# Kernel tuning notes

Hardware: AMD Instinct MI355X
Metric: run time of the kernel (lower is better)

The kernel has to match this reference:

```python
import jax, jax.numpy as jnp
import numpy as np
from jax import lax

NL = 4        # n_layers
V = 32000     # vocab_size
D = 768       # embedding_dim (d_model)
L = 2048      # seq_len
B = 1         # batch
E = 1536      # d_inner = expand * d_model
N = 8         # d_state
R = 48        # dt_rank = ceil(768/16)
K = 3         # d_conv


def rmsnorm(x, w, eps=1e-6):
    return x * w * lax.rsqrt(jnp.mean(x * x, axis=-1, keepdims=True) + eps)


def causal_dwconv(x, w, b):
    # depthwise causal conv1d; x: (B,L,E), w: (K,E), b: (E,)
    xp = jnp.pad(x, ((0, 0), (K - 1, 0), (0, 0)))
    y = sum(xp[:, k:k + x.shape[1], :] * w[k] for k in range(K))
    return y + b


def selective_scan(dt, A, Bm, C, u):
    # dt,u: (B,L,E); A: (E,N); Bm,C: (B,L,N)
    dA = jnp.exp(dt[..., None] * A)                      # (B,L,E,N)
    dBu = dt[..., None] * Bm[:, :, None, :] * u[..., None]  # (B,L,E,N)

    def step(h, xs):
        a, bu, c = xs
        h = a * h + bu                                   # (B,E,N)
        return h, jnp.einsum('ben,bn->be', h, c)

    h0 = jnp.zeros((u.shape[0], E, N), u.dtype)
    _, ys = lax.scan(step, h0, (dA.swapaxes(0, 1), dBu.swapaxes(0, 1), C.swapaxes(0, 1)))
    return ys.swapaxes(0, 1)                             # (B,L,E)


def mamba_block(x, Wi, bi, cw, cb, Wx, Wdt, bdt, Alog, Dsk, Wo, bo):
    xz = x @ Wi + bi                                     # (B,L,2E)
    u, res = jnp.split(xz, 2, axis=-1)
    u = jax.nn.silu(causal_dwconv(u, cw, cb))
    dbl = u @ Wx                                         # (B,L,R+2N)
    dt, Bm, C = dbl[..., :R], dbl[..., R:R + N], dbl[..., R + N:]
    dt = jax.nn.softplus(dt @ Wdt + bdt)                 # (B,L,E)
    A = -jnp.exp(Alog)                                   # (E,N)
    y = selective_scan(dt, A, Bm, C, u) + u * Dsk
    y = y * jax.nn.silu(res)
    return y @ Wo + bo


def setup_inputs() -> dict:
    key = jax.random.key(0)
    ks = jax.random.split(key, 10)
    s = 0.02
    return {
        'inputs': jax.random.randint(ks[0], (B, L), 0, V),
        'emb': jax.random.normal(ks[1], (V, D), jnp.float32) * s,
        'W_in': jax.random.normal(ks[2], (NL, D, 2 * E), jnp.float32) * s,
        'b_in': jnp.zeros((NL, 2 * E), jnp.float32),
        'conv_w': jax.random.normal(ks[3], (NL, K, E), jnp.float32) * s,
        'conv_b': jnp.zeros((NL, E), jnp.float32),
        'W_x': jax.random.normal(ks[4], (NL, E, R + 2 * N), jnp.float32) * s,
        'W_dt': jax.random.normal(ks[5], (NL, R, E), jnp.float32) * s,
        'b_dt': jax.random.normal(ks[6], (NL, E), jnp.float32) * s,
        'A_log': jnp.tile(jnp.log(jnp.arange(1, N + 1, dtype=jnp.float32)), (NL, E, 1)),
        'D_skip': jnp.ones((NL, E), jnp.float32),
        'W_out': jax.random.normal(ks[7], (NL, E, D), jnp.float32) * s,
        'b_out': jnp.zeros((NL, D), jnp.float32),
        'norm_w': jnp.ones((NL, D), jnp.float32),
        'normf_w': jnp.ones((D,), jnp.float32),
        'W_lm': jax.random.normal(ks[8], (D, V), jnp.float32) * s,
    }


def reference(inputs, emb, W_in, b_in, conv_w, conv_b, W_x, W_dt, b_dt, A_log, D_skip, W_out, b_out, norm_w, normf_w, W_lm):
    x = emb[inputs]                                      # (B,L,D)
    for i in range(NL):
        x = x + mamba_block(rmsnorm(x, norm_w[i]), W_in[i], b_in[i], conv_w[i], conv_b[i],
                            W_x[i], W_dt[i], b_dt[i], A_log[i], D_skip[i], W_out[i], b_out[i])
    x = rmsnorm(x, normf_w)
    return x @ W_lm                                      # logits (B,L,V)
```

## Files before the change

### kernel.cpp

```cpp
#include <hip/hip_runtime.h>
#include <hip/hip_bf16.h>
#include <cstdint>
#include <cstddef>

#define L_SEQ 2048
#define DIM   768
#define EDIM  1536
#define NLAY  4
#define NST   8
#define RNK   48
#define VOC   32000
#define NCH   128
#define CHS   16
#define TT    8

typedef __bf16 bf16x8 __attribute__((ext_vector_type(8)));
typedef float  f32x4  __attribute__((ext_vector_type(4)));

typedef __attribute__((address_space(3))) void lds_void;
typedef const __attribute__((address_space(1))) void gbl_void;

__device__ __forceinline__ void gld_lds16(const void* g, void* l) {
    __builtin_amdgcn_global_load_lds((gbl_void*)g, (lds_void*)l, 16, 0, 0);
}

__device__ __forceinline__ float bf2f(__hip_bfloat16 v) { return __bfloat162float(v); }

__global__ __launch_bounds__(256)
void prep_k(const float* __restrict__ W_in, const float* __restrict__ W_out,
            const float* __restrict__ W_lm, const float* __restrict__ W_x,
            __hip_bfloat16* __restrict__ WiT, __hip_bfloat16* __restrict__ WoT,
            __hip_bfloat16* __restrict__ WlmT, __hip_bfloat16* __restrict__ WxT)
{
    __shared__ float tile[32][33];
    int bid = blockIdx.x;
    const float* src; __hip_bfloat16* dst;
    int R, C, c0, r0;
    if (bid < 9216) {
        const int lz = bid / 2304, rem = bid % 2304;
        R = 768; C = 3072; c0 = (rem % 96) * 32; r0 = (rem / 96) * 32;
        src = W_in + (size_t)lz * 768 * 3072; dst = WiT + (size_t)lz * 3072 * 768;
    } else if (bid < 9216 + 4608) {
        bid -= 9216;
        const int lz = bid / 1152, rem = bid % 1152;
        R = 1536; C = 768; c0 = (rem % 24) * 32; r0 = (rem / 24) * 32;
        src = W_out + (size_t)lz * 1536 * 768; dst = WoT + (size_t)lz * 768 * 1536;
    } else if (bid < 9216 + 4608 + 24000) {
        bid -= 9216 + 4608;
        R = 768; C = 32000; c0 = (bid % 1000) * 32; r0 = (bid / 1000) * 32;
        src = W_lm; dst = WlmT;
    } else {
        bid -= 9216 + 4608 + 24000;
        const int lz = bid / 96, rem = bid % 96;
        R = 1536; C = 64; c0 = (rem % 2) * 32; r0 = (rem / 2) * 32;
        src = W_x + (size_t)lz * 1536 * 64; dst = WxT + (size_t)lz * 64 * 1536;
    }
    const int tx = threadIdx.x & 31;
    const int ty = threadIdx.x >> 5;
#pragma unroll
    for (int j = 0; j < 32; j += 8)
        tile[ty + j][tx] = src[(size_t)(r0 + ty + j) * C + c0 + tx];
    __syncthreads();
#pragma unroll
    for (int j = 0; j < 32; j += 8)
        dst[(size_t)(c0 + ty + j) * R + r0 + tx] = __float2bfloat16(tile[tx][ty + j]);
}

template<bool EMB>
__global__ __launch_bounds__(256)
void rmsnorm4_k(const float* __restrict__ src, const float* __restrict__ w,
                __hip_bfloat16* __restrict__ out,
                const int* __restrict__ ids, const float* __restrict__ emb,
                float* __restrict__ xcopy)
{
    const int row  = blockIdx.x * 4 + (threadIdx.x >> 6);
    const int lane = threadIdx.x & 63;
    const float* xr;
    if constexpr (EMB) xr = emb + (size_t)ids[row] * DIM;
    else               xr = src + (size_t)row * DIM;
    float v[12];
    float s = 0.f;
#pragma unroll
    for (int j = 0; j < 12; ++j) { v[j] = xr[lane + j * 64]; s += v[j] * v[j]; }
#pragma unroll
    for (int m = 32; m >= 1; m >>= 1) s += __shfl_xor(s, m, 64);
    const float sc = rsqrtf(s * (1.0f / DIM) + 1e-6f);
    __hip_bfloat16* o = out + (size_t)row * DIM;
#pragma unroll
    for (int j = 0; j < 12; ++j)
        o[lane + j * 64] = __float2bfloat16(v[j] * w[lane + j * 64] * sc);
    if constexpr (EMB) {
        float* xc = xcopy + (size_t)row * DIM;
#pragma unroll
        for (int j = 0; j < 12; ++j) xc[lane + j * 64] = v[j];
    }
}

template<int EPI, int BM, int BN, int BK, typename OT>
__global__ __launch_bounds__(256)
void gemm_bf16(const __hip_bfloat16* __restrict__ A,
               const __hip_bfloat16* __restrict__ BT,
               const float* __restrict__ bias,
               OT* __restrict__ C,
               int M, int N, int K)
{
    constexpr int WM = BM / 2, WN = BN / 2;
    constexpr int MF = WM / 16, NF = WN / 16;
    constexpr int AOPS = BM * BK * 2 / 4096;
    constexpr int BOPS = BN * BK * 2 / 4096;
    constexpr int SOPS = AOPS + BOPS;
    static_assert(SOPS == 3 || SOPS == 4, "vmcnt literal");

    __shared__ __hip_bfloat16 As[2][BM * BK];
    __shared__ __hip_bfloat16 Bs[2][BN * BK];

    const int tid  = threadIdx.x;
    const int lane = tid & 63, wid = tid >> 6;
    const int wr = wid >> 1, wc = wid & 1;

    const int nwg = gridDim.x;
    int wg = blockIdx.x;
    if ((nwg & 7) == 0) wg = (wg & 7) * (nwg >> 3) + (wg >> 3);
    const int mblks = M / BM;
    const int m0 = (wg % mblks) * BM;
    const int n0 = (wg / mblks) * BN;

    f32x4 acc[MF][NF] = {};

    auto stage = [&](int b, int k0) {
#pragma unroll
        for (int i = 0; i < AOPS; ++i) {
            int row, colE;
            if constexpr (BK == 32) { row = i * 64 + (tid >> 2); colE = (((tid & 3) ^ ((tid >> 3) & 3)) << 3); }
            else                    { row = i * 32 + (tid >> 3); colE = (((tid & 7) ^ ((tid >> 3) & 7)) << 3); }
            gld_lds16(A + (size_t)(m0 + row) * K + k0 + colE,
                      (char*)As[b] + i * 4096 + wid * 1024);
        }
#pragma unroll
        for (int i = 0; i < BOPS; ++i) {
            int row, colE;
            if constexpr (BK == 32) { row = i * 64 + (tid >> 2); colE = (((tid & 3) ^ ((tid >> 3) & 3)) << 3); }
            else                    { row = i * 32 + (tid >> 3); colE = (((tid & 7) ^ ((tid >> 3) & 7)) << 3); }
            gld_lds16(BT + (size_t)(n0 + row) * K + k0 + colE,
                      (char*)Bs[b] + i * 4096 + wid * 1024);
        }
    };

    const int NT = K / BK;
    stage(0, 0);

    const int rr   = lane & 15;
    const int kq16 = (lane >> 4) << 4;

    for (int kt = 0; kt < NT; ++kt) {
        const int cur = kt & 1;
        if (kt + 1 < NT) {
            stage(cur ^ 1, (kt + 1) * BK);
            if constexpr (SOPS == 3)
                asm volatile("s_waitcnt vmcnt(3)" ::: "memory");
            else
                asm volatile("s_waitcnt vmcnt(4)" ::: "memory");
        } else {
            asm volatile("s_waitcnt vmcnt(0)" ::: "memory");
        }
        __syncthreads();

        const char* AsB = (const char*)As[cur];
        const char* BsB = (const char*)Bs[cur];
#pragma unroll
        for (int ks = 0; ks < BK / 32; ++ks) {
            bf16x8 af[MF], bfr[NF];
#pragma unroll
            for (int m = 0; m < MF; ++m) {
                const int row = wr * WM + m * 16 + rr;
                const int swz = (BK == 32) ? (((row >> 1) & 3) << 4) : ((row & 7) << 4);
                af[m] = *(const bf16x8*)(AsB + ((row * (BK * 2) + ks * 64 + kq16) ^ swz));
            }
#pragma unroll
            for (int n = 0; n < NF; ++n) {
                const int row = wc * WN + n * 16 + rr;
                const int swz = (BK == 32) ? (((row >> 1) & 3) << 4) : ((row & 7) << 4);
                bfr[n] = *(const bf16x8*)(BsB + ((row * (BK * 2) + ks * 64 + kq16) ^ swz));
            }
#pragma unroll
            for (int m = 0; m < MF; ++m)
#pragma unroll
                for (int n = 0; n < NF; ++n)
                    acc[m][n] = __builtin_amdgcn_mfma_f32_16x16x32_bf16(af[m], bfr[n], acc[m][n], 0, 0, 0);
        }
        __syncthreads();
    }

    const int row0 = m0 + wr * WM + ((lane >> 4) * 4);
    const int col0 = n0 + wc * WN + (lane & 15);
#pragma unroll
    for (int m = 0; m < MF; ++m)
#pragma unroll
        for (int n = 0; n < NF; ++n) {
            const int c = col0 + n * 16;
#pragma unroll
            for (int j = 0; j < 4; ++j) {
                const int r = row0 + m * 16 + j;
                const float v = acc[m][n][j];
                const size_t o = (size_t)r * N + c;
                if constexpr (EPI == 0) {
                    const float z = v + bias[c];
                    if constexpr (__is_same(OT, float)) C[o] = z;
                    else                                C[o] = __float2bfloat16(z);
                } else {
                    C[o] += v + bias[c];
                }
            }
        }
}

__global__ __launch_bounds__(512, 2)
void gemm8_bf16(const __hip_bfloat16* __restrict__ A,
                const __hip_bfloat16* __restrict__ BT,
                float* __restrict__ C,
                int M, int N, int K)
{
    __shared__ uint4 lds_u4[8192];
    char* Aring = (char*)lds_u4;
    char* Bring = (char*)lds_u4 + 65536;

    const int tid  = threadIdx.x;
    const int lane = tid & 63, wid = tid >> 6;
    const int wr = wid >> 2, wc = wid & 3;

    const int nwg = gridDim.x;
    int wg = blockIdx.x;
    if ((nwg & 7) == 0) wg = (wg & 7) * (nwg >> 3) + (wg >> 3);
    const int mblks = M >> 8;
    const int m0 = (wg % mblks) * 256;
    const int n0 = (wg / mblks) * 256;
    const int NT = K >> 6;

    const int rA   = wid * 8 + (lane >> 3);
    const int colE = (((lane & 7) ^ ((lane >> 3) & 7)) << 3);
    const int ldsb = wid * 1024;

    const int rr   = lane & 15;
    const int kq16 = (lane >> 4) << 4;
    const int rbB  = (wc & 1) * 64;

    f32x4 acc[8][4] = {};
    bf16x8 areg[4][2], breg[4][2];

#define STAGE8(SRC, BASE0, TL, TC, H, RING)                                           \
    {                                                                                 \
        const int _slot = ((2 * (TL) + (H)) & 3);                                     \
        const __hip_bfloat16* _g = (SRC) + (size_t)((BASE0) + (H) * 128 + rA) * K     \
                                        + (size_t)(TC) * 64 + colE;                   \
        char* _l = (RING) + _slot * 16384 + ldsb;                                     \
        gld_lds16(_g, _l);                                                            \
        gld_lds16(_g + (size_t)64 * K, _l + 8192);                                    \
    }

#define READ_A8(MH)                                                                   \
    _Pragma("unroll")                                                                 \
    for (int _m = 0; _m < 4; ++_m) {                                                  \
        _Pragma("unroll")                                                             \
        for (int _ks = 0; _ks < 2; ++_ks) {                                           \
            const int _rh = (MH) * 64 + _m * 16 + rr;                                 \
            const int _by = (_rh * 128 + _ks * 64 + kq16) ^ ((_rh & 7) << 4);         \
            areg[_m][_ks] = *(const bf16x8*)(sAp + _by);                              \
        }                                                                             \
    }

#define READ_B8(NH)                                                                   \
    _Pragma("unroll")                                                                 \
    for (int _n = 0; _n < 2; ++_n) {                                                  \
        _Pragma("unroll")                                                             \
        for (int _ks = 0; _ks < 2; ++_ks) {                                           \
            const int _rh = rbB + (NH) * 32 + _n * 16 + rr;                           \
            const int _by = (_rh * 128 + _ks * 64 + kq16) ^ ((_rh & 7) << 4);         \
            breg[(NH) * 2 + _n][_ks] = *(const bf16x8*)(sBp + _by);                   \
        }                                                                             \
    }

#define MFMA_QUAD8(MH, NH)                                                            \
    __builtin_amdgcn_s_setprio(1);                                                    \
    _Pragma("unroll")                                                                 \
    for (int _ks = 0; _ks < 2; ++_ks)                                                 \
        _Pragma("unroll")                                                             \
        for (int _m = 0; _m < 4; ++_m)                                                \
            _Pragma("unroll")                                                         \
            for (int _n = 0; _n < 2; ++_n)                                            \
                acc[(MH) * 4 + _m][(NH) * 2 + _n] =                                   \
                    __builtin_amdgcn_mfma_f32_16x16x32_bf16(                          \
                        areg[_m][_ks], breg[(NH) * 2 + _n][_ks],                      \
                        acc[(MH) * 4 + _m][(NH) * 2 + _n], 0, 0, 0);                  \
    __builtin_amdgcn_s_setprio(0);

    STAGE8(A,  m0, 0, 0, 0, Aring);
    STAGE8(A,  m0, 0, 0, 1, Aring);
    STAGE8(BT, n0, 0, 0, 0, Bring);
    STAGE8(BT, n0, 0, 0, 1, Bring);
    {
        const int t1p = (NT > 1) ? 1 : 0;
        STAGE8(BT, n0, 1, t1p, 0, Bring);
        STAGE8(BT, n0, 1, t1p, 1, Bring);
    }
    asm volatile("s_waitcnt vmcnt(4)" ::: "memory");
    __builtin_amdgcn_s_barrier();

    for (int kt = 0; kt < NT; ++kt) {
        const char* sAp = Aring + (((2 * kt + wr) & 3) << 14);
        const char* sBp = Bring + (((2 * kt + (wc >> 1)) & 3) << 14);
        const int tn1 = (kt + 1 < NT) ? kt + 1 : NT - 1;
        const int tn2 = (kt + 2 < NT) ? kt + 2 : NT - 1;

        READ_A8(0)
        READ_B8(0)
        STAGE8(A, m0, kt + 1, tn1, 0, Aring);
        __builtin_amdgcn_s_barrier();
        MFMA_QUAD8(0, 0)
        __builtin_amdgcn_s_barrier();

        READ_B8(1)
        STAGE8(A, m0, kt + 1, tn1, 1, Aring);
        __builtin_amdgcn_s_barrier();
        MFMA_QUAD8(0, 1)
        __builtin_amdgcn_s_barrier();

        READ_A8(1)
        STAGE8(BT, n0, kt + 2, tn2, 0, Bring);
        __builtin_amdgcn_s_barrier();
        MFMA_QUAD8(1, 0)
        __builtin_amdgcn_s_barrier();

        STAGE8(BT, n0, kt + 2, tn2, 1, Bring);
        __builtin_amdgcn_s_barrier();
        MFMA_QUAD8(1, 1)
        asm volatile("s_waitcnt vmcnt(4)" ::: "memory");
        __builtin_amdgcn_s_barrier();
    }

    const int row0 = m0 + wr * 128 + ((lane >> 4) * 4);
    const int col0 = n0 + wc * 64 + (lane & 15);
#pragma unroll
    for (int m = 0; m < 8; ++m)
#pragma unroll
        for (int n = 0; n < 4; ++n) {
            const int c = col0 + n * 16;
#pragma unroll
            for (int j = 0; j < 4; ++j)
                C[(size_t)(row0 + m * 16 + j) * N + c] = acc[m][n][j];
        }
#undef STAGE8
#undef READ_A8
#undef READ_B8
#undef MFMA_QUAD8
}

__global__ __launch_bounds__(256)
void mid_k(const __hip_bfloat16* __restrict__ xz, const float* __restrict__ cw,
           const float* __restrict__ cb, const __hip_bfloat16* __restrict__ WxT,
           const float* __restrict__ Wdt, const float* __restrict__ bdt,
           __hip_bfloat16* __restrict__ u_f, float* __restrict__ dbl,
           __hip_bfloat16* __restrict__ dtb)
{
    __shared__ __hip_bfloat16 us[TT][EDIM + 8];
    __shared__ float dbs[TT][64];
    const int tid = threadIdx.x;
    const int t0  = blockIdx.x * TT;

#pragma unroll
    for (int j = 0; j < EDIM / 256; ++j) {
        const int e = tid + j * 256;
        const float w0 = cw[e], w1 = cw[EDIM + e], w2 = cw[2 * EDIM + e], b = cb[e];
        float xm2 = (t0 >= 2) ? bf2f(xz[(size_t)(t0 - 2) * (2 * EDIM) + e]) : 0.f;
        float xm1 = (t0 >= 1) ? bf2f(xz[(size_t)(t0 - 1) * (2 * EDIM) + e]) : 0.f;
#pragma unroll
        for (int tt = 0; tt < TT; ++tt) {
            const float xc = bf2f(xz[(size_t)(t0 + tt) * (2 * EDIM) + e]);
            float a = b + w0 * xm2 + w1 * xm1 + w2 * xc;
            a = a / (1.f + __expf(-a));
            const __hip_bfloat16 ab = __float2bfloat16(a);
            us[tt][e] = ab;
            u_f[(size_t)(t0 + tt) * EDIM + e] = ab;
            xm2 = xm1; xm1 = xc;
        }
    }
    __syncthreads();

    {
        const int w = tid >> 6, lane = tid & 63;
        const int rr = lane & 15, kq = (lane >> 4) * 8;
        f32x4 acc = {};
        const __hip_bfloat16* bw = WxT + (size_t)(w * 16 + rr) * EDIM;
#pragma unroll 4
        for (int k0 = 0; k0 < EDIM; k0 += 32) {
            const bf16x8 af  = *(const bf16x8*)(&us[rr & (TT - 1)][k0 + kq]);
            const bf16x8 bfr = *(const bf16x8*)(bw + k0 + kq);
            acc = __builtin_amdgcn_mfma_f32_16x16x32_bf16(af, bfr, acc, 0, 0, 0);
        }
        const int nn = w * 16 + (lane & 15);
#pragma unroll
        for (int j = 0; j < 4; ++j) {
            const int tt2 = (lane >> 4) * 4 + j;
            if (tt2 < TT) {
                dbs[tt2][nn] = acc[j];
                dbl[(size_t)(t0 + tt2) * 64 + nn] = acc[j];
            }
        }
    }
    __syncthreads();

#pragma unroll 1
    for (int j = 0; j < EDIM / 256; ++j) {
        const int e = tid + j * 256;
        float wreg[RNK];
#pragma unroll
        for (int r = 0; r < RNK; ++r) wreg[r] = Wdt[(size_t)r * EDIM + e];
        const float b = bdt[e];
#pragma unroll 1
        for (int tt = 0; tt < TT; ++tt) {
            float acc = b;
#pragma unroll
            for (int r = 0; r < RNK; ++r) acc += dbs[tt][r] * wreg[r];
            const float ax = fabsf(acc);
            dtb[(size_t)(t0 + tt) * EDIM + e] =
                __float2bfloat16(fmaxf(acc, 0.f) + log1pf(__expf(-ax)));
        }
    }
}

__global__ __launch_bounds__(64)
void scanA_k(const __hip_bfloat16* __restrict__ dt, const __hip_bfloat16* __restrict__ u_f,
             const float* __restrict__ dbl, const float* __restrict__ alog,
             __hip_bfloat16* __restrict__ Pb, __hip_bfloat16* __restrict__ Hb)
{
    const int lane = threadIdx.x;
    const int e  = blockIdx.x * 64 + lane;
    const int c  = blockIdx.y;
    const int t0 = c * CHS;
    __shared__ float BC[CHS][16];
    if (lane < CHS) {
        const float4* s4 = (const float4*)(dbl + (size_t)(t0 + lane) * 64 + 48);
        float4* d4 = (float4*)(&BC[lane][0]);
        d4[0] = s4[0]; d4[1] = s4[1]; d4[2] = s4[2]; d4[3] = s4[3];
    }
    __syncthreads();
    float A8[NST], h[NST], P[NST];
#pragma unroll
    for (int n = 0; n < NST; ++n) {
        A8[n] = -__expf(alog[(size_t)e * NST + n]);
        h[n] = 0.f; P[n] = 1.f;
    }
    float pdt[8], pu[8];
#pragma unroll
    for (int j = 0; j < 8; ++j) {
        pdt[j] = bf2f(dt [(size_t)(t0 + j) * EDIM + e]);
        pu [j] = bf2f(u_f[(size_t)(t0 + j) * EDIM + e]);
    }
    for (int tb = 0; tb < CHS; tb += 8) {
        float cdt[8], cu[8];
#pragma unroll
        for (int j = 0; j < 8; ++j) { cdt[j] = pdt[j]; cu[j] = pu[j]; }
        if (tb + 8 < CHS) {
#pragma unroll
            for (int j = 0; j < 8; ++j) {
                pdt[j] = bf2f(dt [(size_t)(t0 + tb + 8 + j) * EDIM + e]);
                pu [j] = bf2f(u_f[(size_t)(t0 + tb + 8 + j) * EDIM + e]);
            }
        }
#pragma unroll
        for (int j = 0; j < 8; ++j) {
            const float du = cdt[j] * cu[j];
#pragma unroll
            for (int n = 0; n < NST; ++n) {
                const float dA = __expf(cdt[j] * A8[n]);
                h[n] = dA * h[n] + du * BC[tb + j][n];
                P[n] *= dA;
            }
        }
    }
    const size_t o = ((size_t)c * EDIM + e) * NST;
    bf16x8 pv, hv;
#pragma unroll
    for (int n = 0; n < NST; ++n) { pv[n] = (__bf16)P[n]; hv[n] = (__bf16)h[n]; }
    *(bf16x8*)(Pb + o) = pv;
    *(bf16x8*)(Hb + o) = hv;
}

__global__ __launch_bounds__(256)
void scanB_k(const __hip_bfloat16* __restrict__ Pb, const __hip_bfloat16* __restrict__ Hb,
             float* __restrict__ Hin)
{
    const int idx = blockIdx.x * 256 + threadIdx.x;
    float h = 0.f;
#pragma unroll 8
    for (int c = 0; c < NCH; ++c) {
        const size_t o = (size_t)c * EDIM * NST + idx;
        Hin[o] = h;
        h = bf2f(Pb[o]) * h + bf2f(Hb[o]);
    }
}

__global__ __launch_bounds__(64)
void scanC_k(const __hip_bfloat16* __restrict__ dt, const __hip_bfloat16* __restrict__ u_f,
             const float* __restrict__ dbl, const float* __restrict__ alog,
             const float* __restrict__ Hin, const float* __restrict__ Dsk,
             const __hip_bfloat16* __restrict__ xz, __hip_bfloat16* __restrict__ ybf)
{
    const int lane = threadIdx.x;
    const int e  = blockIdx.x * 64 + lane;
    const int c  = blockIdx.y;
    const int t0 = c * CHS;
    __shared__ float BC[CHS][16];
    if (lane < CHS) {
        const float4* s4 = (const float4*)(dbl + (size_t)(t0 + lane) * 64 + 48);
        float4* d4 = (float4*)(&BC[lane][0]);
        d4[0] = s4[0]; d4[1] = s4[1]; d4[2] = s4[2]; d4[3] = s4[3];
    }
    __syncthreads();
    float A8[NST], h[NST];
#pragma unroll
    for (int n = 0; n < NST; ++n) {
        A8[n] = -__expf(alog[(size_t)e * NST + n]);
        h[n]  = Hin[(size_t)c * EDIM * NST + (size_t)e * NST + n];
    }
    const float Dv = Dsk[e];
    float pdt[8], pu[8], pr[8];
#pragma unroll
    for (int j = 0; j < 8; ++j) {
        pdt[j] = bf2f(dt [(size_t)(t0 + j) * EDIM + e]);
        pu [j] = bf2f(u_f[(size_t)(t0 + j) * EDIM + e]);
        pr [j] = bf2f(xz [(size_t)(t0 + j) * (2 * EDIM) + EDIM + e]);
    }
    for (int tb = 0; tb < CHS; tb += 8) {
        float cdt[8], cu[8], cr[8];
#pragma unroll
        for (int j = 0; j < 8; ++j) { cdt[j] = pdt[j]; cu[j] = pu[j]; cr[j] = pr[j]; }
        if (tb + 8 < CHS) {
#pragma unroll
            for (int j = 0; j < 8; ++j) {
                pdt[j] = bf2f(dt [(size_t)(t0 + tb + 8 + j) * EDIM + e]);
                pu [j] = bf2f(u_f[(size_t)(t0 + tb + 8 + j) * EDIM + e]);
                pr [j] = bf2f(xz [(size_t)(t0 + tb + 8 + j) * (2 * EDIM) + EDIM + e]);
            }
        }
#pragma unroll
        for (int j = 0; j < 8; ++j) {
            const float du = cdt[j] * cu[j];
            float y = 0.f;
#pragma unroll
            for (int n = 0; n < NST; ++n) {
                const float dA = __expf(cdt[j] * A8[n]);
                h[n] = dA * h[n] + du * BC[tb + j][n];
                y += h[n] * BC[tb + j][8 + n];
            }
            y += cu[j] * Dv;
            y *= cr[j] / (1.f + __expf(-cr[j]));
            ybf[(size_t)(t0 + tb + j) * EDIM + e] = __float2bfloat16(y);
        }
    }
}

extern "C" void kernel_launch(void* const* d_in, const int* in_sizes, int n_in,
                              void* d_out, int out_size, void* d_ws, size_t ws_size,
                              hipStream_t stream)
{
    const int*   ids     = (const int*)  d_in[0];
    const float* emb     = (const float*)d_in[1];
    const float* W_in    = (const float*)d_in[2];
    const float* b_in    = (const float*)d_in[3];
    const float* conv_w  = (const float*)d_in[4];
    const float* conv_b  = (const float*)d_in[5];
    const float* W_x     = (const float*)d_in[6];
    const float* W_dt    = (const float*)d_in[7];
    const float* b_dt    = (const float*)d_in[8];
    const float* A_log   = (const float*)d_in[9];
    const float* D_skip  = (const float*)d_in[10];
    const float* W_out   = (const float*)d_in[11];
    const float* b_out   = (const float*)d_in[12];
    const float* norm_w  = (const float*)d_in[13];
    const float* normf_w = (const float*)d_in[14];
    const float* W_lm    = (const float*)d_in[15];
    float* out = (float*)d_out;
    (void)in_sizes; (void)n_in; (void)out_size; (void)ws_size;

    char* ws = (char*)d_ws;
    size_t off = 0;
    auto alloc = [&](size_t b) -> void* {
        void* p = ws + off;
        off += (b + 255) & ~(size_t)255;
        return p;
    };
    __hip_bfloat16* WiT  = (__hip_bfloat16*)alloc((size_t)NLAY * 3072 * 768 * 2);
    __hip_bfloat16* WoT  = (__hip_bfloat16*)alloc((size_t)NLAY * 768 * 1536 * 2);
    __hip_bfloat16* WlmT = (__hip_bfloat16*)alloc((size_t)VOC * 768 * 2);
    __hip_bfloat16* WxT  = (__hip_bfloat16*)alloc((size_t)NLAY * 64 * EDIM * 2);
    float* x    = (float*)alloc((size_t)L_SEQ * DIM * 4);
    __hip_bfloat16* xn  = (__hip_bfloat16*)alloc((size_t)L_SEQ * DIM * 2);
    __hip_bfloat16* xz  = (__hip_bfloat16*)alloc((size_t)L_SEQ * 2 * EDIM * 2);
    __hip_bfloat16* u_f = (__hip_bfloat16*)alloc((size_t)L_SEQ * EDIM * 2);
    float* dblb = (float*)alloc((size_t)L_SEQ * 64 * 4);
    __hip_bfloat16* dtb = (__hip_bfloat16*)alloc((size_t)L_SEQ * EDIM * 2);
    __hip_bfloat16* ybf = (__hip_bfloat16*)alloc((size_t)L_SEQ * EDIM * 2);
    __hip_bfloat16* Pb  = (__hip_bfloat16*)alloc((size_t)NCH * EDIM * NST * 2);
    __hip_bfloat16* Hb  = (__hip_bfloat16*)alloc((size_t)NCH * EDIM * NST * 2);
    float* Hin  = (float*)alloc((size_t)NCH * EDIM * NST * 4);

    prep_k<<<dim3(9216 + 4608 + 24000 + 384), 256, 0, stream>>>(
        W_in, W_out, W_lm, W_x, WiT, WoT, WlmT, WxT);

    rmsnorm4_k<true><<<dim3(L_SEQ / 4), 256, 0, stream>>>(
        nullptr, norm_w, xn, ids, emb, x);

    for (int l = 0; l < NLAY; ++l) {
        if (l > 0)
            rmsnorm4_k<false><<<dim3(L_SEQ / 4), 256, 0, stream>>>(
                x, norm_w + l * DIM, xn, nullptr, nullptr, nullptr);
        gemm_bf16<0, 128, 64, 32, __hip_bfloat16>
            <<<dim3((L_SEQ / 128) * (3072 / 64)), 256, 0, stream>>>(
            xn, WiT + (size_t)l * 3072 * 768, b_in + l * 2 * EDIM, xz, L_SEQ, 2 * EDIM, DIM);
        mid_k<<<dim3(L_SEQ / TT), 256, 0, stream>>>(
            xz, conv_w + l * 3 * EDIM, conv_b + l * EDIM,
            WxT + (size_t)l * 64 * EDIM,
            W_dt + (size_t)l * RNK * EDIM, b_dt + l * EDIM,
            u_f, dblb, dtb);
        scanA_k<<<dim3(EDIM / 64, NCH), 64, 0, stream>>>(
            dtb, u_f, dblb, A_log + (size_t)l * EDIM * NST, Pb, Hb);
        scanB_k<<<dim3(EDIM * NST / 256), 256, 0, stream>>>(Pb, Hb, Hin);
        scanC_k<<<dim3(EDIM / 64, NCH), 64, 0, stream>>>(
            dtb, u_f, dblb, A_log + (size_t)l * EDIM * NST, Hin, D_skip + l * EDIM, xz, ybf);
        gemm_bf16<1, 64, 64, 64, float>
            <<<dim3((L_SEQ / 64) * (768 / 64)), 256, 0, stream>>>(
            ybf, WoT + (size_t)l * 768 * 1536, b_out + l * DIM, x, L_SEQ, DIM, EDIM);
    }

    rmsnorm4_k<false><<<dim3(L_SEQ / 4), 256, 0, stream>>>(
        x, normf_w, xn, nullptr, nullptr, nullptr);
    gemm8_bf16<<<dim3((VOC / 256) * (L_SEQ / 256)), 512, 0, stream>>>(
        xn, WlmT, out, L_SEQ, VOC, DIM);
}
```

Before: 692.6 us.

## Parallelize chunk-carry scan with wave shuffles and widen in-proj GEMM K tile

The serial loop over 128 chunks in the inter-chunk state pass becomes a wave-level parallel prefix scan. Each lane composes two chunks' affine (P,H) pairs, then the lanes combine them with shuffle-up steps, and the grid grows to one wave per state element. The cost removed is the long dependent chain of 128 sequential load-multiply-add steps. Separately, the input-projection GEMM moves from a K tile of 32 to 64, which changes the count of staged loads per stage and needs a new vmcnt(6) wait case. Memory access in the scan is now strided across chunks per wave, so coalescing gets worse.

```diff
diff --git a/kernel.cpp b/kernel.cpp
--- a/kernel.cpp
+++ b/kernel.cpp
@@ -109,7 +109,7 @@
     constexpr int AOPS = BM * BK * 2 / 4096;
     constexpr int BOPS = BN * BK * 2 / 4096;
     constexpr int SOPS = AOPS + BOPS;
-    static_assert(SOPS == 3 || SOPS == 4, "vmcnt literal");
+    static_assert(SOPS == 3 || SOPS == 4 || SOPS == 6, "vmcnt literal");
 
     __shared__ __hip_bfloat16 As[2][BM * BK];
     __shared__ __hip_bfloat16 Bs[2][BN * BK];
@@ -158,8 +158,10 @@
             stage(cur ^ 1, (kt + 1) * BK);
             if constexpr (SOPS == 3)
                 asm volatile("s_waitcnt vmcnt(3)" ::: "memory");
+            else if constexpr (SOPS == 4)
+                asm volatile("s_waitcnt vmcnt(4)" ::: "memory");
             else
-                asm volatile("s_waitcnt vmcnt(4)" ::: "memory");
+                asm volatile("s_waitcnt vmcnt(6)" ::: "memory");
         } else {
             asm volatile("s_waitcnt vmcnt(0)" ::: "memory");
         }
@@ -489,14 +491,31 @@
 void scanB_k(const __hip_bfloat16* __restrict__ Pb, const __hip_bfloat16* __restrict__ Hb,
              float* __restrict__ Hin)
 {
-    const int idx = blockIdx.x * 256 + threadIdx.x;
-    float h = 0.f;
-#pragma unroll 8
-    for (int c = 0; c < NCH; ++c) {
-        const size_t o = (size_t)c * EDIM * NST + idx;
-        Hin[o] = h;
-        h = bf2f(Pb[o]) * h + bf2f(Hb[o]);
-    }
+    const int lane = threadIdx.x & 63;
+    const int w    = threadIdx.x >> 6;
+    const int idx  = blockIdx.x * 4 + w;
+    const size_t S = (size_t)EDIM * NST;
+    const size_t o0 = (size_t)(2 * lane)     * S + idx;
+    const size_t o1 = (size_t)(2 * lane + 1) * S + idx;
+    const float p0 = bf2f(Pb[o0]);
+    const float q0 = bf2f(Hb[o0]);
+    const float p1 = bf2f(Pb[o1]);
+    const float q1 = bf2f(Hb[o1]);
+    float Pl = p0 * p1;
+    float Ql = p1 * q0 + q1;
+#pragma unroll
+    for (int d = 1; d < 64; d <<= 1) {
+        const float Pp = __shfl_up(Pl, d, 64);
+        const float Qp = __shfl_up(Ql, d, 64);
+        if (lane >= d) {
+            Ql = Pl * Qp + Ql;
+            Pl = Pp * Pl;
+        }
+    }
+    float Qe = __shfl_up(Ql, 1, 64);
+    if (lane == 0) Qe = 0.f;
+    Hin[o0] = Qe;
+    Hin[o1] = p0 * Qe + q0;
 }
 
 __global__ __launch_bounds__(64)
@@ -614,7 +633,7 @@
         if (l > 0)
             rmsnorm4_k<false><<<dim3(L_SEQ / 4), 256, 0, stream>>>(
                 x, norm_w + l * DIM, xn, nullptr, nullptr, nullptr);
-        gemm_bf16<0, 128, 64, 32, __hip_bfloat16>
+        gemm_bf16<0, 128, 64, 64, __hip_bfloat16>
             <<<dim3((L_SEQ / 128) * (3072 / 64)), 256, 0, stream>>>(
             xn, WiT + (size_t)l * 3072 * 768, b_in + l * 2 * EDIM, xz, L_SEQ, 2 * EDIM, DIM);
         mid_k<<<dim3(L_SEQ / TT), 256, 0, stream>>>(
@@ -624,7 +643,7 @@
             u_f, dblb, dtb);
         scanA_k<<<dim3(EDIM / 64, NCH), 64, 0, stream>>>(
             dtb, u_f, dblb, A_log + (size_t)l * EDIM * NST, Pb, Hb);
-        scanB_k<<<dim3(EDIM * NST / 256), 256, 0, stream>>>(Pb, Hb, Hin);
+        scanB_k<<<dim3(EDIM * NST / 4), 256, 0, stream>>>(Pb, Hb, Hin);
         scanC_k<<<dim3(EDIM / 64, NCH), 64, 0, stream>>>(
             dtb, u_f, dblb, A_log + (size_t)l * EDIM * NST, Hin, D_skip + l * EDIM, xz, ybf);
         gemm_bf16<1, 64, 64, 64, float>
```

Result: no change. 696.8 us (+0.6%).
